# Kernel optimization log

Measured on AMD Instinct MI355X. Metric: run time of the kernel, lower is better.

Reference implementation:

```python
import jax, jax.numpy as jnp
import numpy as np

B, H, W, C = 32, 512, 512, 3


def dct2_matrix(N):
    # Orthonormal DCT-II basis: D[k, n] = s_k * sqrt(2/N) * cos(pi*(2n+1)*k/(2N))
    n = np.arange(N)
    k = n[:, None]
    D = np.cos(np.pi * (2 * n[None, :] + 1) * k / (2.0 * N)) * np.sqrt(2.0 / N)
    D[0, :] *= 1.0 / np.sqrt(2.0)  # ortho scaling of DC row
    return jnp.asarray(D, dtype=jnp.float32)


def setup_inputs() -> dict:
    key = jax.random.key(0)
    x = jax.random.normal(key, (B, H, W, C), dtype=jnp.float32)
    return {"x": x}


def reference(x) -> jnp.ndarray:
    # 2D DCT-II (ortho) along height and width, channels untouched.
    Dh = dct2_matrix(x.shape[1])  # [H, H]
    Dw = dct2_matrix(x.shape[2])  # [W, W]
    y = jnp.einsum('kh,bhwc->bkwc', Dh, x)   # DCT over height
    y = jnp.einsum('lw,bkwc->bklc', Dw, y)   # DCT over width
    return y
```

## Files before the change

### kernel.cpp

```cpp
#include <hip/hip_runtime.h>
#include <stdint.h>


typedef __bf16 bf16_t;
typedef bf16_t bf16x8 __attribute__((ext_vector_type(8)));
typedef float  f32x4  __attribute__((ext_vector_type(4)));

__device__ __forceinline__ uint32_t f2bf(float f) {
    union { float f; uint32_t u; } v; v.f = f;
    uint32_t r = v.u + 0x7fffu + ((v.u >> 16) & 1u);
    return r >> 16;
}

__device__ __forceinline__ f32x4 mfma16(bf16x8 a, bf16x8 b, f32x4 c) {
    return __builtin_amdgcn_mfma_f32_16x16x32_bf16(a, b, c, 0, 0, 0);
}

__device__ __forceinline__ void load_lds16(const void* g, void* l) {
    __builtin_amdgcn_global_load_lds(
        (const __attribute__((address_space(1))) uint32_t*)g,
        (__attribute__((address_space(3))) uint32_t*)l, 16, 0, 0);
}

__global__ __launch_bounds__(256) void gen_dct(uint16_t* __restrict__ Dbf) {
    int idx = blockIdx.x * 256 + threadIdx.x;
    int k = idx >> 9, h = idx & 511;
    int phase = ((2 * h + 1) * k) & 2047;
    float ang = (float)phase * 3.0679615757712823e-3f;
    float s = (k == 0) ? 0.04419417382415922f : 0.0625f;
    Dbf[idx] = (uint16_t)f2bf(__cosf(ang) * s);
}

__global__ __launch_bounds__(256, 3) void pass1(const float* __restrict__ x,
                                                const uint16_t* __restrict__ Dbf,
                                                uint16_t* __restrict__ Y) {
    __shared__ __align__(16) uint16_t Alds[128 * 32];
    __shared__ __align__(16) uint16_t Blds[96 * 32];
    const int t = threadIdx.x;
    const int lane = t & 63, wv = t >> 6;
    const int nt = blockIdx.x;
    const int mt = blockIdx.y;
    const int b  = blockIdx.z;
    const float* xb = x + (size_t)b * (512 * 1536);

    const int jl = t % 96;
    const int hh = t / 96;
    const int wl = jl / 3, cc = jl - 3 * wl;
    const int ncol = cc * 32 + ((wl >> 1) + ((wl & 1) << 4));
    const int xv = (ncol >> 1) & 3;
    const int jg = nt * 96 + jl;

    f32x4 acc[2][6] = {};

    for (int kt = 0; kt < 16; ++kt) {
        __syncthreads();
        {
            int q = t;
            load_lds16(Dbf + (size_t)(mt * 128 + (q >> 2)) * 512 + kt * 32 + (q & 3) * 8,
                       Alds + q * 8);
            int q2 = t + 256;
            load_lds16(Dbf + (size_t)(mt * 128 + (q2 >> 2)) * 512 + kt * 32 + (q2 & 3) * 8,
                       Alds + q2 * 8);
        }
        if (t < 192) {
            const float* src = xb + (size_t)(kt * 32 + hh * 16) * 1536 + jg;
            float v[16];
#pragma unroll
            for (int r = 0; r < 16; ++r) v[r] = src[(size_t)r * 1536];
            uint32_t p[8];
#pragma unroll
            for (int i = 0; i < 8; ++i)
                p[i] = f2bf(v[2 * i]) | (f2bf(v[2 * i + 1]) << 16);
            *(uint4*)&Blds[ncol * 32 + (((hh * 2 + 0) ^ xv) << 3)] =
                make_uint4(p[0], p[1], p[2], p[3]);
            *(uint4*)&Blds[ncol * 32 + (((hh * 2 + 1) ^ xv) << 3)] =
                make_uint4(p[4], p[5], p[6], p[7]);
        }
        __syncthreads();

        bf16x8 aq[2];
#pragma unroll
        for (int i = 0; i < 2; ++i)
            aq[i] = *(bf16x8*)&Alds[((wv * 2 + i) * 16 + (lane & 15)) * 32 + ((lane >> 4) << 3)];
#pragma unroll
        for (int tt = 0; tt < 6; ++tt) {
            int col = tt * 16 + (lane & 15);
            bf16x8 bq = *(bf16x8*)&Blds[col * 32 + (((lane >> 4) ^ ((col >> 1) & 3)) << 3)];
            acc[0][tt] = mfma16(aq[0], bq, acc[0][tt]);
            acc[1][tt] = mfma16(aq[1], bq, acc[1][tt]);
        }
    }

    const int wg = nt * 32 + 2 * (lane & 15);
#pragma unroll
    for (int i = 0; i < 2; ++i) {
        int kg = mt * 128 + (wv * 2 + i) * 16 + ((lane >> 4) << 2);
#pragma unroll
        for (int c = 0; c < 3; ++c)
#pragma unroll
            for (int r = 0; r < 4; ++r) {
                uint32_t pk = f2bf(acc[i][2 * c][r]) | (f2bf(acc[i][2 * c + 1][r]) << 16);
                *(uint32_t*)&Y[(size_t)b * 786432 + (size_t)(kg + r) * 1536 + c * 512 + wg] = pk;
            }
    }
}

__global__ __launch_bounds__(256, 3) void pass2(const uint16_t* __restrict__ Y,
                                                const uint16_t* __restrict__ Dbf,
                                                float* __restrict__ out) {
    __shared__ __align__(16) char smem[96 * 130 * 4];
    uint16_t* Alds = (uint16_t*)smem;
    uint16_t* Blds = (uint16_t*)(smem + 6144);
    float*    Elds = (float*)smem;
    const int t = threadIdx.x;
    const int lane = t & 63, wv = t >> 6;
    const int lt = blockIdx.x;
    const int mt = blockIdx.y;
    const int b  = blockIdx.z;
    const size_t yb = (size_t)b * 786432;

    f32x4 acc[6][2] = {};

    for (int kt = 0; kt < 16; ++kt) {
        __syncthreads();
        {
            int q = t;
            load_lds16(Y + yb + (size_t)(mt * 96 + (q >> 2)) * 512 + kt * 32 + (q & 3) * 8,
                       Alds + q * 8);
            if (t < 128) {
                int q2 = 256 + t;
                load_lds16(Y + yb + (size_t)(mt * 96 + (q2 >> 2)) * 512 + kt * 32 + (q2 & 3) * 8,
                           Alds + q2 * 8);
            }
            int q3 = t;
            load_lds16(Dbf + (size_t)(lt * 128 + (q3 >> 2)) * 512 + kt * 32 + (q3 & 3) * 8,
                       Blds + q3 * 8);
            int q4 = t + 256;
            load_lds16(Dbf + (size_t)(lt * 128 + (q4 >> 2)) * 512 + kt * 32 + (q4 & 3) * 8,
                       Blds + q4 * 8);
        }
        __syncthreads();

        bf16x8 bq[2];
#pragma unroll
        for (int p = 0; p < 2; ++p)
            bq[p] = *(bf16x8*)&Blds[((wv * 2 + p) * 16 + (lane & 15)) * 32 + ((lane >> 4) << 3)];
#pragma unroll
        for (int tt = 0; tt < 6; ++tt) {
            bf16x8 aq = *(bf16x8*)&Alds[(tt * 16 + (lane & 15)) * 32 + ((lane >> 4) << 3)];
            acc[tt][0] = mfma16(aq, bq[0], acc[tt][0]);
            acc[tt][1] = mfma16(aq, bq[1], acc[tt][1]);
        }
    }

    __syncthreads();
#pragma unroll
    for (int tt = 0; tt < 6; ++tt)
#pragma unroll
        for (int p = 0; p < 2; ++p) {
            int m = tt * 16 + ((lane >> 4) << 2);
            int ll = (wv * 2 + p) * 16 + (lane & 15);
#pragma unroll
            for (int r = 0; r < 4; ++r)
                Elds[(m + r) * 130 + ll] = acc[tt][p][r];
        }
    __syncthreads();

    const int kloc = t >> 3, sub = t & 7;
    size_t ob = (size_t)b * 786432 + (size_t)(mt * 32 + kloc) * 1536 + lt * 384 + sub * 48;
#pragma unroll
    for (int q = 0; q < 12; ++q) {
        int o0 = sub * 48 + q * 4;
        float4 v;
        v.x = Elds[(kloc * 3 + ((o0 + 0) % 3)) * 130 + (o0 + 0) / 3];
        v.y = Elds[(kloc * 3 + ((o0 + 1) % 3)) * 130 + (o0 + 1) / 3];
        v.z = Elds[(kloc * 3 + ((o0 + 2) % 3)) * 130 + (o0 + 2) / 3];
        v.w = Elds[(kloc * 3 + ((o0 + 3) % 3)) * 130 + (o0 + 3) / 3];
        *(float4*)&out[ob + q * 4] = v;
    }
}

extern "C" void kernel_launch(void* const* d_in, const int* in_sizes, int n_in,
                              void* d_out, int out_size, void* d_ws, size_t ws_size,
                              hipStream_t stream) {
    (void)in_sizes; (void)n_in; (void)out_size; (void)ws_size;
    const float* x = (const float*)d_in[0];
    float* out = (float*)d_out;
    uint16_t* Dbf = (uint16_t*)d_ws;
    uint16_t* Y   = (uint16_t*)d_ws + 512 * 512;

    gen_dct<<<1024, 256, 0, stream>>>(Dbf);
    dim3 g1(16, 4, 32);
    pass1<<<g1, 256, 0, stream>>>(x, Dbf, Y);
    dim3 g2(4, 16, 32);
    pass2<<<g2, 256, 0, stream>>>(Y, Dbf, out);
}
```

Baseline: 292.4 us.

## Double-buffer LDS tiles in both DCT GEMM passes with swizzled A loads

Both GEMM passes now keep two LDS buffers and prefetch the next K-tile while MFMAs run on the current one, so only one barrier per iteration remains. The global-to-LDS copies for the DCT matrix and Y tiles use an XOR swizzle to cut LDS bank conflicts on fragment reads. Pass2's epilogue is split into two halves so its staging area fits the smaller shared buffer, which allows occupancy to rise from 3 to 4 blocks. In exchange there is more register pressure from holding prefetched x values across the MFMA loop, and the epilogue needs extra barriers.

```diff
diff --git a/kernel.cpp b/kernel.cpp
--- a/kernel.cpp
+++ b/kernel.cpp
@@ -31,11 +31,11 @@
     Dbf[idx] = (uint16_t)f2bf(__cosf(ang) * s);
 }
 
-__global__ __launch_bounds__(256, 3) void pass1(const float* __restrict__ x,
+__global__ __launch_bounds__(256, 4) void pass1(const float* __restrict__ x,
                                                 const uint16_t* __restrict__ Dbf,
                                                 uint16_t* __restrict__ Y) {
-    __shared__ __align__(16) uint16_t Alds[128 * 32];
-    __shared__ __align__(16) uint16_t Blds[96 * 32];
+    __shared__ __align__(16) uint16_t Alds[2][128 * 32];
+    __shared__ __align__(16) uint16_t Blds[2][96 * 32];
     const int t = threadIdx.x;
     const int lane = t & 63, wv = t >> 6;
     const int nt = blockIdx.x;
@@ -43,52 +43,79 @@
     const int b  = blockIdx.z;
     const float* xb = x + (size_t)b * (512 * 1536);
 
+    const int q0 = t, q1 = t + 256;
+    const int m0 = q0 >> 2, i0 = (q0 & 3) ^ ((m0 >> 1) & 3);
+    const int m1 = q1 >> 2, i1 = (q1 & 3) ^ ((m1 >> 1) & 3);
+    const uint16_t* Asrc0 = Dbf + (size_t)(mt * 128 + m0) * 512 + i0 * 8;
+    const uint16_t* Asrc1 = Dbf + (size_t)(mt * 128 + m1) * 512 + i1 * 8;
+
     const int jl = t % 96;
     const int hh = t / 96;
     const int wl = jl / 3, cc = jl - 3 * wl;
     const int ncol = cc * 32 + ((wl >> 1) + ((wl & 1) << 4));
     const int xv = (ncol >> 1) & 3;
     const int jg = nt * 96 + jl;
+    const float* xsrc = xb + (size_t)(hh * 16) * 1536 + jg;
 
     f32x4 acc[2][6] = {};
+    float v[16];
+
+    load_lds16(Asrc0, &Alds[0][q0 * 8]);
+    load_lds16(Asrc1, &Alds[0][q1 * 8]);
+    if (t < 192) {
+#pragma unroll
+        for (int r = 0; r < 16; ++r) v[r] = xsrc[(size_t)r * 1536];
+        uint32_t p[8];
+#pragma unroll
+        for (int i = 0; i < 8; ++i)
+            p[i] = f2bf(v[2 * i]) | (f2bf(v[2 * i + 1]) << 16);
+        *(uint4*)&Blds[0][ncol * 32 + (((hh * 2 + 0) ^ xv) << 3)] =
+            make_uint4(p[0], p[1], p[2], p[3]);
+        *(uint4*)&Blds[0][ncol * 32 + (((hh * 2 + 1) ^ xv) << 3)] =
+            make_uint4(p[4], p[5], p[6], p[7]);
+    }
+    __syncthreads();
 
     for (int kt = 0; kt < 16; ++kt) {
-        __syncthreads();
-        {
-            int q = t;
-            load_lds16(Dbf + (size_t)(mt * 128 + (q >> 2)) * 512 + kt * 32 + (q & 3) * 8,
-                       Alds + q * 8);
-            int q2 = t + 256;
-            load_lds16(Dbf + (size_t)(mt * 128 + (q2 >> 2)) * 512 + kt * 32 + (q2 & 3) * 8,
-                       Alds + q2 * 8);
-        }
-        if (t < 192) {
-            const float* src = xb + (size_t)(kt * 32 + hh * 16) * 1536 + jg;
-            float v[16];
-#pragma unroll
-            for (int r = 0; r < 16; ++r) v[r] = src[(size_t)r * 1536];
+        const int cur = kt & 1, nxt = cur ^ 1;
+
+        if (kt < 15) {
+            load_lds16(Asrc0 + (kt + 1) * 32, &Alds[nxt][q0 * 8]);
+            load_lds16(Asrc1 + (kt + 1) * 32, &Alds[nxt][q1 * 8]);
+            if (t < 192) {
+                const float* s = xsrc + (size_t)(kt + 1) * 32 * 1536;
+#pragma unroll
+                for (int r = 0; r < 16; ++r) v[r] = s[(size_t)r * 1536];
+            }
+        }
+
+        bf16x8 aq[2];
+#pragma unroll
+        for (int i = 0; i < 2; ++i) {
+            int row = (wv * 2 + i) * 16 + (lane & 15);
+            aq[i] = *(bf16x8*)&Alds[cur][row * 32 +
+                        (((lane >> 4) ^ ((row >> 1) & 3)) << 3)];
+        }
+#pragma unroll
+        for (int tt = 0; tt < 6; ++tt) {
+            int col = tt * 16 + (lane & 15);
+            bf16x8 bq = *(bf16x8*)&Blds[cur][col * 32 +
+                        (((lane >> 4) ^ ((col >> 1) & 3)) << 3)];
+            acc[0][tt] = mfma16(aq[0], bq, acc[0][tt]);
+            acc[1][tt] = mfma16(aq[1], bq, acc[1][tt]);
+        }
+
+        if (kt < 15 && t < 192) {
             uint32_t p[8];
 #pragma unroll
             for (int i = 0; i < 8; ++i)
                 p[i] = f2bf(v[2 * i]) | (f2bf(v[2 * i + 1]) << 16);
-            *(uint4*)&Blds[ncol * 32 + (((hh * 2 + 0) ^ xv) << 3)] =
+            *(uint4*)&Blds[nxt][ncol * 32 + (((hh * 2 + 0) ^ xv) << 3)] =
                 make_uint4(p[0], p[1], p[2], p[3]);
-            *(uint4*)&Blds[ncol * 32 + (((hh * 2 + 1) ^ xv) << 3)] =
+            *(uint4*)&Blds[nxt][ncol * 32 + (((hh * 2 + 1) ^ xv) << 3)] =
                 make_uint4(p[4], p[5], p[6], p[7]);
         }
         __syncthreads();
-
-        bf16x8 aq[2];
-#pragma unroll
-        for (int i = 0; i < 2; ++i)
-            aq[i] = *(bf16x8*)&Alds[((wv * 2 + i) * 16 + (lane & 15)) * 32 + ((lane >> 4) << 3)];
-#pragma unroll
-        for (int tt = 0; tt < 6; ++tt) {
-            int col = tt * 16 + (lane & 15);
-            bf16x8 bq = *(bf16x8*)&Blds[col * 32 + (((lane >> 4) ^ ((col >> 1) & 3)) << 3)];
-            acc[0][tt] = mfma16(aq[0], bq, acc[0][tt]);
-            acc[1][tt] = mfma16(aq[1], bq, acc[1][tt]);
-        }
     }
 
     const int wg = nt * 32 + 2 * (lane & 15);
@@ -105,13 +132,10 @@
     }
 }
 
-__global__ __launch_bounds__(256, 3) void pass2(const uint16_t* __restrict__ Y,
+__global__ __launch_bounds__(256, 4) void pass2(const uint16_t* __restrict__ Y,
                                                 const uint16_t* __restrict__ Dbf,
                                                 float* __restrict__ out) {
-    __shared__ __align__(16) char smem[96 * 130 * 4];
-    uint16_t* Alds = (uint16_t*)smem;
-    uint16_t* Blds = (uint16_t*)(smem + 6144);
-    float*    Elds = (float*)smem;
+    __shared__ __align__(16) char smem[28672];
     const int t = threadIdx.x;
     const int lane = t & 63, wv = t >> 6;
     const int lt = blockIdx.x;
@@ -119,64 +143,87 @@
     const int b  = blockIdx.z;
     const size_t yb = (size_t)b * 786432;
 
+    const int qa0 = t;
+    const int ma0 = qa0 >> 2, ia0 = (qa0 & 3) ^ ((ma0 >> 1) & 3);
+    const int qa1 = t + 256;
+    const int ma1 = qa1 >> 2, ia1 = (qa1 & 3) ^ ((ma1 >> 1) & 3);
+    const int mb0 = ma0, ib0 = ia0;
+    const int mb1 = ma1, ib1 = ia1;
+
+    const uint16_t* As0 = Y + yb + (size_t)(mt * 96 + ma0) * 512 + ia0 * 8;
+    const uint16_t* As1 = Y + yb + (size_t)(mt * 96 + ma1) * 512 + ia1 * 8;
+    const uint16_t* Bs0 = Dbf + (size_t)(lt * 128 + mb0) * 512 + ib0 * 8;
+    const uint16_t* Bs1 = Dbf + (size_t)(lt * 128 + mb1) * 512 + ib1 * 8;
+
     f32x4 acc[6][2] = {};
 
+    auto stage = [&](int kt, int buf) {
+        uint16_t* Al = (uint16_t*)(smem + buf * 14336);
+        uint16_t* Bl = (uint16_t*)(smem + buf * 14336 + 6144);
+        load_lds16(As0 + kt * 32, Al + qa0 * 8);
+        if (t < 128) load_lds16(As1 + kt * 32, Al + qa1 * 8);
+        load_lds16(Bs0 + kt * 32, Bl + qa0 * 8);
+        load_lds16(Bs1 + kt * 32, Bl + qa1 * 8);
+    };
+
+    stage(0, 0);
+    __syncthreads();
+
     for (int kt = 0; kt < 16; ++kt) {
-        __syncthreads();
-        {
-            int q = t;
-            load_lds16(Y + yb + (size_t)(mt * 96 + (q >> 2)) * 512 + kt * 32 + (q & 3) * 8,
-                       Alds + q * 8);
-            if (t < 128) {
-                int q2 = 256 + t;
-                load_lds16(Y + yb + (size_t)(mt * 96 + (q2 >> 2)) * 512 + kt * 32 + (q2 & 3) * 8,
-                           Alds + q2 * 8);
-            }
-            int q3 = t;
-            load_lds16(Dbf + (size_t)(lt * 128 + (q3 >> 2)) * 512 + kt * 32 + (q3 & 3) * 8,
-                       Blds + q3 * 8);
-            int q4 = t + 256;
-            load_lds16(Dbf + (size_t)(lt * 128 + (q4 >> 2)) * 512 + kt * 32 + (q4 & 3) * 8,
-                       Blds + q4 * 8);
-        }
-        __syncthreads();
+        const int cur = kt & 1;
+        if (kt < 15) stage(kt + 1, cur ^ 1);
+
+        const uint16_t* Al = (const uint16_t*)(smem + cur * 14336);
+        const uint16_t* Bl = (const uint16_t*)(smem + cur * 14336 + 6144);
 
         bf16x8 bq[2];
 #pragma unroll
-        for (int p = 0; p < 2; ++p)
-            bq[p] = *(bf16x8*)&Blds[((wv * 2 + p) * 16 + (lane & 15)) * 32 + ((lane >> 4) << 3)];
+        for (int p = 0; p < 2; ++p) {
+            int row = (wv * 2 + p) * 16 + (lane & 15);
+            bq[p] = *(bf16x8*)&Bl[row * 32 +
+                        (((lane >> 4) ^ ((row >> 1) & 3)) << 3)];
+        }
 #pragma unroll
         for (int tt = 0; tt < 6; ++tt) {
-            bf16x8 aq = *(bf16x8*)&Alds[(tt * 16 + (lane & 15)) * 32 + ((lane >> 4) << 3)];
+            int row = tt * 16 + (lane & 15);
+            bf16x8 aq = *(bf16x8*)&Al[row * 32 +
+                        (((lane >> 4) ^ ((row >> 1) & 3)) << 3)];
             acc[tt][0] = mfma16(aq, bq[0], acc[tt][0]);
             acc[tt][1] = mfma16(aq, bq[1], acc[tt][1]);
         }
-    }
-
-    __syncthreads();
-#pragma unroll
-    for (int tt = 0; tt < 6; ++tt)
-#pragma unroll
-        for (int p = 0; p < 2; ++p) {
-            int m = tt * 16 + ((lane >> 4) << 2);
-            int ll = (wv * 2 + p) * 16 + (lane & 15);
-#pragma unroll
-            for (int r = 0; r < 4; ++r)
-                Elds[(m + r) * 130 + ll] = acc[tt][p][r];
-        }
-    __syncthreads();
-
+        __syncthreads();
+    }
+
+    float* El = (float*)smem;
     const int kloc = t >> 3, sub = t & 7;
-    size_t ob = (size_t)b * 786432 + (size_t)(mt * 32 + kloc) * 1536 + lt * 384 + sub * 48;
-#pragma unroll
-    for (int q = 0; q < 12; ++q) {
-        int o0 = sub * 48 + q * 4;
-        float4 v;
-        v.x = Elds[(kloc * 3 + ((o0 + 0) % 3)) * 130 + (o0 + 0) / 3];
-        v.y = Elds[(kloc * 3 + ((o0 + 1) % 3)) * 130 + (o0 + 1) / 3];
-        v.z = Elds[(kloc * 3 + ((o0 + 2) % 3)) * 130 + (o0 + 2) / 3];
-        v.w = Elds[(kloc * 3 + ((o0 + 3) % 3)) * 130 + (o0 + 3) / 3];
-        *(float4*)&out[ob + q * 4] = v;
+#pragma unroll
+    for (int hf = 0; hf < 2; ++hf) {
+        __syncthreads();
+        if ((wv >> 1) == hf) {
+#pragma unroll
+            for (int tt = 0; tt < 6; ++tt)
+#pragma unroll
+                for (int p = 0; p < 2; ++p) {
+                    int m = tt * 16 + ((lane >> 4) << 2);
+                    int lc = ((wv & 1) * 2 + p) * 16 + (lane & 15);
+#pragma unroll
+                    for (int r = 0; r < 4; ++r)
+                        El[(m + r) * 65 + lc] = acc[tt][p][r];
+                }
+        }
+        __syncthreads();
+        size_t ob = (size_t)b * 786432 + (size_t)(mt * 32 + kloc) * 1536 +
+                    lt * 384 + hf * 192 + sub * 24;
+#pragma unroll
+        for (int q = 0; q < 6; ++q) {
+            int o0 = hf * 192 + sub * 24 + q * 4;
+            float4 v;
+            v.x = El[(kloc * 3 + ((o0 + 0) % 3)) * 65 + ((o0 + 0) / 3 - hf * 64)];
+            v.y = El[(kloc * 3 + ((o0 + 1) % 3)) * 65 + ((o0 + 1) / 3 - hf * 64)];
+            v.z = El[(kloc * 3 + ((o0 + 2) % 3)) * 65 + ((o0 + 2) / 3 - hf * 64)];
+            v.w = El[(kloc * 3 + ((o0 + 3) % 3)) * 65 + ((o0 + 3) / 3 - hf * 64)];
+            *(float4*)&out[ob + q * 4] = v;
+        }
     }
 }
 
```

Result: faster. 277.6 us (-5.1%).

## Double output tile per block in both DCT passes and swizzle LDS operands

Applied to the files above, without the earlier changes.

Each block of pass1 and pass2 now computes two 128-row tiles of the DCT basis output instead of one, so every loaded tile of x (pass1) or Y (pass2) is reused across twice as many MFMAs. The grid shrinks by half in the tiled dimension. XOR swizzles are added to the A/B LDS layouts to cut bank conflicts, and load addresses are hoisted out of the k loop. Pass2's epilogue is split into four smaller LDS staging rounds to fit the smaller shared buffer. The cost is doubled accumulator registers, which may lower occupancy, and fewer blocks in flight.

```diff
diff --git a/kernel.cpp b/kernel.cpp
--- a/kernel.cpp
+++ b/kernel.cpp
@@ -34,36 +34,43 @@
 __global__ __launch_bounds__(256, 3) void pass1(const float* __restrict__ x,
                                                 const uint16_t* __restrict__ Dbf,
                                                 uint16_t* __restrict__ Y) {
-    __shared__ __align__(16) uint16_t Alds[128 * 32];
+    __shared__ __align__(16) uint16_t Alds[256 * 32];
     __shared__ __align__(16) uint16_t Blds[96 * 32];
     const int t = threadIdx.x;
     const int lane = t & 63, wv = t >> 6;
     const int nt = blockIdx.x;
-    const int mt = blockIdx.y;
+    const int mp = blockIdx.y;
     const int b  = blockIdx.z;
     const float* xb = x + (size_t)b * (512 * 1536);
+
+    const int q0 = t, q1 = t + 256, q2 = t + 512, q3 = t + 768;
+    const int m0 = q0 >> 2, i0 = (q0 & 3) ^ ((m0 >> 1) & 3);
+    const int m1 = q1 >> 2, i1 = (q1 & 3) ^ ((m1 >> 1) & 3);
+    const int m2 = q2 >> 2, i2 = (q2 & 3) ^ ((m2 >> 1) & 3);
+    const int m3 = q3 >> 2, i3 = (q3 & 3) ^ ((m3 >> 1) & 3);
+    const uint16_t* As0 = Dbf + (size_t)(mp * 256 + m0) * 512 + i0 * 8;
+    const uint16_t* As1 = Dbf + (size_t)(mp * 256 + m1) * 512 + i1 * 8;
+    const uint16_t* As2 = Dbf + (size_t)(mp * 256 + m2) * 512 + i2 * 8;
+    const uint16_t* As3 = Dbf + (size_t)(mp * 256 + m3) * 512 + i3 * 8;
 
     const int jl = t % 96;
     const int hh = t / 96;
     const int wl = jl / 3, cc = jl - 3 * wl;
     const int ncol = cc * 32 + ((wl >> 1) + ((wl & 1) << 4));
-    const int xv = (ncol >> 1) & 3;
+    const int xv = ((ncol >> 1) ^ (ncol >> 3) ^ (ncol >> 5)) & 3;
     const int jg = nt * 96 + jl;
-
-    f32x4 acc[2][6] = {};
+    const float* xsrc = xb + (size_t)(hh * 16) * 1536 + jg;
+
+    f32x4 acc[2][2][6] = {};
 
     for (int kt = 0; kt < 16; ++kt) {
         __syncthreads();
-        {
-            int q = t;
-            load_lds16(Dbf + (size_t)(mt * 128 + (q >> 2)) * 512 + kt * 32 + (q & 3) * 8,
-                       Alds + q * 8);
-            int q2 = t + 256;
-            load_lds16(Dbf + (size_t)(mt * 128 + (q2 >> 2)) * 512 + kt * 32 + (q2 & 3) * 8,
-                       Alds + q2 * 8);
-        }
+        load_lds16(As0 + kt * 32, Alds + q0 * 8);
+        load_lds16(As1 + kt * 32, Alds + q1 * 8);
+        load_lds16(As2 + kt * 32, Alds + q2 * 8);
+        load_lds16(As3 + kt * 32, Alds + q3 * 8);
         if (t < 192) {
-            const float* src = xb + (size_t)(kt * 32 + hh * 16) * 1536 + jg;
+            const float* src = xsrc + (size_t)kt * 32 * 1536;
             float v[16];
 #pragma unroll
             for (int r = 0; r < 16; ++r) v[r] = src[(size_t)r * 1536];
@@ -78,105 +85,140 @@
         }
         __syncthreads();
 
-        bf16x8 aq[2];
-#pragma unroll
-        for (int i = 0; i < 2; ++i)
-            aq[i] = *(bf16x8*)&Alds[((wv * 2 + i) * 16 + (lane & 15)) * 32 + ((lane >> 4) << 3)];
+        bf16x8 aq[2][2];
+#pragma unroll
+        for (int mtk = 0; mtk < 2; ++mtk)
+#pragma unroll
+            for (int i = 0; i < 2; ++i) {
+                int row = mtk * 128 + (wv * 2 + i) * 16 + (lane & 15);
+                aq[mtk][i] = *(const bf16x8*)&Alds[row * 32 +
+                                (((lane >> 4) ^ ((row >> 1) & 3)) << 3)];
+            }
 #pragma unroll
         for (int tt = 0; tt < 6; ++tt) {
             int col = tt * 16 + (lane & 15);
-            bf16x8 bq = *(bf16x8*)&Blds[col * 32 + (((lane >> 4) ^ ((col >> 1) & 3)) << 3)];
-            acc[0][tt] = mfma16(aq[0], bq, acc[0][tt]);
-            acc[1][tt] = mfma16(aq[1], bq, acc[1][tt]);
+            int xr = ((col >> 1) ^ (col >> 3) ^ (col >> 5)) & 3;
+            bf16x8 bq = *(const bf16x8*)&Blds[col * 32 + (((lane >> 4) ^ xr) << 3)];
+#pragma unroll
+            for (int mtk = 0; mtk < 2; ++mtk) {
+                acc[mtk][0][tt] = mfma16(aq[mtk][0], bq, acc[mtk][0][tt]);
+                acc[mtk][1][tt] = mfma16(aq[mtk][1], bq, acc[mtk][1][tt]);
+            }
         }
     }
 
     const int wg = nt * 32 + 2 * (lane & 15);
 #pragma unroll
-    for (int i = 0; i < 2; ++i) {
-        int kg = mt * 128 + (wv * 2 + i) * 16 + ((lane >> 4) << 2);
-#pragma unroll
-        for (int c = 0; c < 3; ++c)
-#pragma unroll
-            for (int r = 0; r < 4; ++r) {
-                uint32_t pk = f2bf(acc[i][2 * c][r]) | (f2bf(acc[i][2 * c + 1][r]) << 16);
-                *(uint32_t*)&Y[(size_t)b * 786432 + (size_t)(kg + r) * 1536 + c * 512 + wg] = pk;
-            }
-    }
+    for (int mtk = 0; mtk < 2; ++mtk)
+#pragma unroll
+        for (int i = 0; i < 2; ++i) {
+            int kg = mp * 256 + mtk * 128 + (wv * 2 + i) * 16 + ((lane >> 4) << 2);
+#pragma unroll
+            for (int c = 0; c < 3; ++c)
+#pragma unroll
+                for (int r = 0; r < 4; ++r) {
+                    uint32_t pk = f2bf(acc[mtk][i][2 * c][r]) |
+                                  (f2bf(acc[mtk][i][2 * c + 1][r]) << 16);
+                    *(uint32_t*)&Y[(size_t)b * 786432 + (size_t)(kg + r) * 1536 +
+                                   c * 512 + wg] = pk;
+                }
+        }
 }
 
 __global__ __launch_bounds__(256, 3) void pass2(const uint16_t* __restrict__ Y,
                                                 const uint16_t* __restrict__ Dbf,
                                                 float* __restrict__ out) {
-    __shared__ __align__(16) char smem[96 * 130 * 4];
+    __shared__ __align__(16) char smem[24960];
     uint16_t* Alds = (uint16_t*)smem;
     uint16_t* Blds = (uint16_t*)(smem + 6144);
-    float*    Elds = (float*)smem;
+    float*    El   = (float*)smem;
     const int t = threadIdx.x;
     const int lane = t & 63, wv = t >> 6;
-    const int lt = blockIdx.x;
+    const int lp = blockIdx.x;
     const int mt = blockIdx.y;
     const int b  = blockIdx.z;
     const size_t yb = (size_t)b * 786432;
 
-    f32x4 acc[6][2] = {};
+    const int q0 = t, q1 = t + 256, q2 = t + 512, q3 = t + 768;
+    const int m0 = q0 >> 2, i0 = (q0 & 3) ^ ((m0 >> 1) & 3);
+    const int m1 = q1 >> 2, i1 = (q1 & 3) ^ ((m1 >> 1) & 3);
+    const int m2 = q2 >> 2, i2 = (q2 & 3) ^ ((m2 >> 1) & 3);
+    const int m3 = q3 >> 2, i3 = (q3 & 3) ^ ((m3 >> 1) & 3);
+
+    const uint16_t* Ys0 = Y + yb + (size_t)(mt * 96 + m0) * 512 + i0 * 8;
+    const uint16_t* Ys1 = Y + yb + (size_t)(mt * 96 + m1) * 512 + i1 * 8;
+    const uint16_t* Ds0 = Dbf + (size_t)(lp * 256 + m0) * 512 + i0 * 8;
+    const uint16_t* Ds1 = Dbf + (size_t)(lp * 256 + m1) * 512 + i1 * 8;
+    const uint16_t* Ds2 = Dbf + (size_t)(lp * 256 + m2) * 512 + i2 * 8;
+    const uint16_t* Ds3 = Dbf + (size_t)(lp * 256 + m3) * 512 + i3 * 8;
+
+    f32x4 acc[6][2][2] = {};
 
     for (int kt = 0; kt < 16; ++kt) {
         __syncthreads();
-        {
-            int q = t;
-            load_lds16(Y + yb + (size_t)(mt * 96 + (q >> 2)) * 512 + kt * 32 + (q & 3) * 8,
-                       Alds + q * 8);
-            if (t < 128) {
-                int q2 = 256 + t;
-                load_lds16(Y + yb + (size_t)(mt * 96 + (q2 >> 2)) * 512 + kt * 32 + (q2 & 3) * 8,
-                           Alds + q2 * 8);
-            }
-            int q3 = t;
-            load_lds16(Dbf + (size_t)(lt * 128 + (q3 >> 2)) * 512 + kt * 32 + (q3 & 3) * 8,
-                       Blds + q3 * 8);
-            int q4 = t + 256;
-            load_lds16(Dbf + (size_t)(lt * 128 + (q4 >> 2)) * 512 + kt * 32 + (q4 & 3) * 8,
-                       Blds + q4 * 8);
-        }
-        __syncthreads();
-
-        bf16x8 bq[2];
-#pragma unroll
-        for (int p = 0; p < 2; ++p)
-            bq[p] = *(bf16x8*)&Blds[((wv * 2 + p) * 16 + (lane & 15)) * 32 + ((lane >> 4) << 3)];
+        load_lds16(Ys0 + kt * 32, Alds + q0 * 8);
+        if (t < 128) load_lds16(Ys1 + kt * 32, Alds + q1 * 8);
+        load_lds16(Ds0 + kt * 32, Blds + q0 * 8);
+        load_lds16(Ds1 + kt * 32, Blds + q1 * 8);
+        load_lds16(Ds2 + kt * 32, Blds + q2 * 8);
+        load_lds16(Ds3 + kt * 32, Blds + q3 * 8);
+        __syncthreads();
+
+        bf16x8 bq[2][2];
+#pragma unroll
+        for (int lt2 = 0; lt2 < 2; ++lt2)
+#pragma unroll
+            for (int p = 0; p < 2; ++p) {
+                int row = lt2 * 128 + (wv * 2 + p) * 16 + (lane & 15);
+                bq[lt2][p] = *(const bf16x8*)&Blds[row * 32 +
+                                (((lane >> 4) ^ ((row >> 1) & 3)) << 3)];
+            }
 #pragma unroll
         for (int tt = 0; tt < 6; ++tt) {
-            bf16x8 aq = *(bf16x8*)&Alds[(tt * 16 + (lane & 15)) * 32 + ((lane >> 4) << 3)];
-            acc[tt][0] = mfma16(aq, bq[0], acc[tt][0]);
-            acc[tt][1] = mfma16(aq, bq[1], acc[tt][1]);
+            int row = tt * 16 + (lane & 15);
+            bf16x8 aq = *(const bf16x8*)&Alds[row * 32 +
+                            (((lane >> 4) ^ ((row >> 1) & 3)) << 3)];
+#pragma unroll
+            for (int lt2 = 0; lt2 < 2; ++lt2) {
+                acc[tt][0][lt2] = mfma16(aq, bq[lt2][0], acc[tt][0][lt2]);
+                acc[tt][1][lt2] = mfma16(aq, bq[lt2][1], acc[tt][1][lt2]);
+            }
         }
     }
 
-    __syncthreads();
-#pragma unroll
-    for (int tt = 0; tt < 6; ++tt)
-#pragma unroll
-        for (int p = 0; p < 2; ++p) {
-            int m = tt * 16 + ((lane >> 4) << 2);
-            int ll = (wv * 2 + p) * 16 + (lane & 15);
-#pragma unroll
-            for (int r = 0; r < 4; ++r)
-                Elds[(m + r) * 130 + ll] = acc[tt][p][r];
-        }
-    __syncthreads();
-
     const int kloc = t >> 3, sub = t & 7;
-    size_t ob = (size_t)b * 786432 + (size_t)(mt * 32 + kloc) * 1536 + lt * 384 + sub * 48;
-#pragma unroll
-    for (int q = 0; q < 12; ++q) {
-        int o0 = sub * 48 + q * 4;
-        float4 v;
-        v.x = Elds[(kloc * 3 + ((o0 + 0) % 3)) * 130 + (o0 + 0) / 3];
-        v.y = Elds[(kloc * 3 + ((o0 + 1) % 3)) * 130 + (o0 + 1) / 3];
-        v.z = Elds[(kloc * 3 + ((o0 + 2) % 3)) * 130 + (o0 + 2) / 3];
-        v.w = Elds[(kloc * 3 + ((o0 + 3) % 3)) * 130 + (o0 + 3) / 3];
-        *(float4*)&out[ob + q * 4] = v;
+#pragma unroll
+    for (int lt2 = 0; lt2 < 2; ++lt2) {
+        const int lte = lp * 2 + lt2;
+#pragma unroll
+        for (int hf = 0; hf < 2; ++hf) {
+            __syncthreads();
+            if ((wv >> 1) == hf) {
+#pragma unroll
+                for (int tt = 0; tt < 6; ++tt)
+#pragma unroll
+                    for (int p = 0; p < 2; ++p) {
+                        int m = tt * 16 + ((lane >> 4) << 2);
+                        int lc = ((wv & 1) * 2 + p) * 16 + (lane & 15);
+#pragma unroll
+                        for (int r = 0; r < 4; ++r)
+                            El[(m + r) * 65 + lc] = acc[tt][p][lt2][r];
+                    }
+            }
+            __syncthreads();
+            size_t ob = (size_t)b * 786432 + (size_t)(mt * 32 + kloc) * 1536 +
+                        lte * 384 + hf * 192 + sub * 24;
+#pragma unroll
+            for (int q = 0; q < 6; ++q) {
+                int o0 = hf * 192 + sub * 24 + q * 4;
+                float4 v;
+                v.x = El[(kloc * 3 + ((o0 + 0) % 3)) * 65 + ((o0 + 0) / 3 - hf * 64)];
+                v.y = El[(kloc * 3 + ((o0 + 1) % 3)) * 65 + ((o0 + 1) / 3 - hf * 64)];
+                v.z = El[(kloc * 3 + ((o0 + 2) % 3)) * 65 + ((o0 + 2) / 3 - hf * 64)];
+                v.w = El[(kloc * 3 + ((o0 + 3) % 3)) * 65 + ((o0 + 3) / 3 - hf * 64)];
+                *(float4*)&out[ob + q * 4] = v;
+            }
+        }
     }
 }
 
@@ -190,8 +232,8 @@
     uint16_t* Y   = (uint16_t*)d_ws + 512 * 512;
 
     gen_dct<<<1024, 256, 0, stream>>>(Dbf);
-    dim3 g1(16, 4, 32);
+    dim3 g1(16, 2, 32);
     pass1<<<g1, 256, 0, stream>>>(x, Dbf, Y);
-    dim3 g2(4, 16, 32);
+    dim3 g2(2, 16, 32);
     pass2<<<g2, 256, 0, stream>>>(Y, Dbf, out);
 }
```

New measurement: 292.5 us. About the same (+0.0%).

## Split fp32-to-bf16 transpose out of GEMM1 and enlarge MFMA tiles to 512 threads

Applied to the files above, without the earlier changes.

Adds a separate transpose kernel that converts x to bf16 and lays it out with height contiguous, so the first GEMM can stream both operands with direct global-to-LDS loads. Both GEMMs move to 512-thread blocks with larger tiles (128x256 and 96x256), a K-step of 64 and XOR-swizzled LDS. The output epilogue is staged in two rounds through LDS. The extra transpose kernel adds a full read and write of the input plus another launch, and Xt falls back to aliasing the output buffer when the workspace is too small.

```diff
diff --git a/kernel.cpp b/kernel.cpp
--- a/kernel.cpp
+++ b/kernel.cpp
@@ -31,167 +31,220 @@
     Dbf[idx] = (uint16_t)f2bf(__cosf(ang) * s);
 }
 
-__global__ __launch_bounds__(256, 3) void pass1(const float* __restrict__ x,
+__global__ __launch_bounds__(256) void xpose(const float* __restrict__ x,
+                                             uint16_t* __restrict__ Xt) {
+    const int jt = blockIdx.x, hb = blockIdx.y, b = blockIdx.z;
+    const int t = threadIdx.x;
+    const int jl = t & 127, hh = t >> 7;
+    const int jg = jt * 128 + jl;
+    const int w = jg / 3, c = jg - 3 * w;
+    const int wr = ((w >> 8) << 8) + ((w & 255) >> 1) + ((w & 1) << 7);
+    const int jr = c * 512 + wr;
+    const float* src = x + (size_t)b * 786432 +
+                       (size_t)(hb * 32 + hh * 16) * 1536 + jg;
+    float v[16];
+#pragma unroll
+    for (int r = 0; r < 16; ++r) v[r] = src[(size_t)r * 1536];
+    uint32_t p[8];
+#pragma unroll
+    for (int i = 0; i < 8; ++i)
+        p[i] = f2bf(v[2 * i]) | (f2bf(v[2 * i + 1]) << 16);
+    size_t dst = ((size_t)b * 1536 + jr) * 512 + hb * 32 + hh * 16;
+    *(uint4*)&Xt[dst]     = make_uint4(p[0], p[1], p[2], p[3]);
+    *(uint4*)&Xt[dst + 8] = make_uint4(p[4], p[5], p[6], p[7]);
+}
+
+__global__ __launch_bounds__(512, 2) void gemm1(const uint16_t* __restrict__ Xt,
                                                 const uint16_t* __restrict__ Dbf,
                                                 uint16_t* __restrict__ Y) {
-    __shared__ __align__(16) uint16_t Alds[128 * 32];
-    __shared__ __align__(16) uint16_t Blds[96 * 32];
+    __shared__ __align__(16) uint16_t Al[128 * 64];
+    __shared__ __align__(16) uint16_t Bl[256 * 64];
     const int t = threadIdx.x;
     const int lane = t & 63, wv = t >> 6;
+    const int wm = wv >> 2, wn = wv & 3;
     const int nt = blockIdx.x;
     const int mt = blockIdx.y;
     const int b  = blockIdx.z;
-    const float* xb = x + (size_t)b * (512 * 1536);
-
-    const int jl = t % 96;
-    const int hh = t / 96;
-    const int wl = jl / 3, cc = jl - 3 * wl;
-    const int ncol = cc * 32 + ((wl >> 1) + ((wl & 1) << 4));
-    const int xv = (ncol >> 1) & 3;
-    const int jg = nt * 96 + jl;
-
-    f32x4 acc[2][6] = {};
-
-    for (int kt = 0; kt < 16; ++kt) {
-        __syncthreads();
-        {
-            int q = t;
-            load_lds16(Dbf + (size_t)(mt * 128 + (q >> 2)) * 512 + kt * 32 + (q & 3) * 8,
-                       Alds + q * 8);
-            int q2 = t + 256;
-            load_lds16(Dbf + (size_t)(mt * 128 + (q2 >> 2)) * 512 + kt * 32 + (q2 & 3) * 8,
-                       Alds + q2 * 8);
-        }
-        if (t < 192) {
-            const float* src = xb + (size_t)(kt * 32 + hh * 16) * 1536 + jg;
-            float v[16];
-#pragma unroll
-            for (int r = 0; r < 16; ++r) v[r] = src[(size_t)r * 1536];
-            uint32_t p[8];
-#pragma unroll
-            for (int i = 0; i < 8; ++i)
-                p[i] = f2bf(v[2 * i]) | (f2bf(v[2 * i + 1]) << 16);
-            *(uint4*)&Blds[ncol * 32 + (((hh * 2 + 0) ^ xv) << 3)] =
-                make_uint4(p[0], p[1], p[2], p[3]);
-            *(uint4*)&Blds[ncol * 32 + (((hh * 2 + 1) ^ xv) << 3)] =
-                make_uint4(p[4], p[5], p[6], p[7]);
-        }
-        __syncthreads();
-
-        bf16x8 aq[2];
-#pragma unroll
-        for (int i = 0; i < 2; ++i)
-            aq[i] = *(bf16x8*)&Alds[((wv * 2 + i) * 16 + (lane & 15)) * 32 + ((lane >> 4) << 3)];
-#pragma unroll
-        for (int tt = 0; tt < 6; ++tt) {
-            int col = tt * 16 + (lane & 15);
-            bf16x8 bq = *(bf16x8*)&Blds[col * 32 + (((lane >> 4) ^ ((col >> 1) & 3)) << 3)];
-            acc[0][tt] = mfma16(aq[0], bq, acc[0][tt]);
-            acc[1][tt] = mfma16(aq[1], bq, acc[1][tt]);
-        }
-    }
-
-    const int wg = nt * 32 + 2 * (lane & 15);
-#pragma unroll
-    for (int i = 0; i < 2; ++i) {
-        int kg = mt * 128 + (wv * 2 + i) * 16 + ((lane >> 4) << 2);
-#pragma unroll
-        for (int c = 0; c < 3; ++c)
+
+    const int qa0 = t, qa1 = t + 512;
+    const int ma0 = qa0 >> 3, ga0 = (qa0 & 7) ^ (ma0 & 7);
+    const int ma1 = qa1 >> 3, ga1 = (qa1 & 7) ^ (ma1 & 7);
+    const uint16_t* As0 = Dbf + (size_t)(mt * 128 + ma0) * 512 + ga0 * 8;
+    const uint16_t* As1 = Dbf + (size_t)(mt * 128 + ma1) * 512 + ga1 * 8;
+    const uint16_t* Bs[4];
+    int qb[4];
+#pragma unroll
+    for (int i = 0; i < 4; ++i) {
+        qb[i] = t + 512 * i;
+        int mb = qb[i] >> 3, gb = (qb[i] & 7) ^ (mb & 7);
+        Bs[i] = Xt + ((size_t)b * 1536 + nt * 256 + mb) * 512 + gb * 8;
+    }
+
+    f32x4 acc[4][4] = {};
+
+    for (int kt = 0; kt < 8; ++kt) {
+        __syncthreads();
+        load_lds16(As0 + kt * 64, Al + qa0 * 8);
+        load_lds16(As1 + kt * 64, Al + qa1 * 8);
+#pragma unroll
+        for (int i = 0; i < 4; ++i)
+            load_lds16(Bs[i] + kt * 64, Bl + qb[i] * 8);
+        __syncthreads();
+
+#pragma unroll
+        for (int ks = 0; ks < 2; ++ks) {
+            bf16x8 aq[4], bq[4];
+#pragma unroll
+            for (int mf = 0; mf < 4; ++mf) {
+                int row = wm * 64 + mf * 16 + (lane & 15);
+                int sl = (ks * 4 + (lane >> 4)) ^ (row & 7);
+                aq[mf] = *(const bf16x8*)&Al[row * 64 + sl * 8];
+            }
+#pragma unroll
+            for (int f = 0; f < 4; ++f) {
+                int col = (wn + 4 * f) * 16 + (lane & 15);
+                int sl = (ks * 4 + (lane >> 4)) ^ (col & 7);
+                bq[f] = *(const bf16x8*)&Bl[col * 64 + sl * 8];
+            }
+#pragma unroll
+            for (int mf = 0; mf < 4; ++mf)
+#pragma unroll
+                for (int f = 0; f < 4; ++f)
+                    acc[mf][f] = mfma16(aq[mf], bq[f], acc[mf][f]);
+        }
+    }
+
+    const int cch = nt >> 1, whalf = nt & 1;
+#pragma unroll
+    for (int mf = 0; mf < 4; ++mf)
+#pragma unroll
+        for (int fp = 0; fp < 2; ++fp) {
+            int kbase = mt * 128 + wm * 64 + mf * 16 + ((lane >> 4) << 2);
+            int u = wn + 4 * fp;
+            int w = whalf * 256 + 2 * (u * 16 + (lane & 15));
 #pragma unroll
             for (int r = 0; r < 4; ++r) {
-                uint32_t pk = f2bf(acc[i][2 * c][r]) | (f2bf(acc[i][2 * c + 1][r]) << 16);
-                *(uint32_t*)&Y[(size_t)b * 786432 + (size_t)(kg + r) * 1536 + c * 512 + wg] = pk;
-            }
-    }
-}
-
-__global__ __launch_bounds__(256, 3) void pass2(const uint16_t* __restrict__ Y,
+                uint32_t pk = f2bf(acc[mf][fp][r]) |
+                              (f2bf(acc[mf][fp + 2][r]) << 16);
+                *(uint32_t*)&Y[(size_t)b * 786432 + (size_t)(kbase + r) * 1536 +
+                               cch * 512 + w] = pk;
+            }
+        }
+}
+
+__global__ __launch_bounds__(512, 4) void gemm2(const uint16_t* __restrict__ Y,
                                                 const uint16_t* __restrict__ Dbf,
                                                 float* __restrict__ out) {
-    __shared__ __align__(16) char smem[96 * 130 * 4];
-    uint16_t* Alds = (uint16_t*)smem;
-    uint16_t* Blds = (uint16_t*)(smem + 6144);
-    float*    Elds = (float*)smem;
+    __shared__ __align__(16) char smem[49408];
+    uint16_t* Al = (uint16_t*)smem;
+    uint16_t* Bl = (uint16_t*)(smem + 12288);
+    float*    El = (float*)smem;
     const int t = threadIdx.x;
     const int lane = t & 63, wv = t >> 6;
-    const int lt = blockIdx.x;
-    const int mt = blockIdx.y;
+    const int wm = wv >> 2, wn = wv & 3;
+    const int mt = blockIdx.x;
+    const int lt = blockIdx.y;
     const int b  = blockIdx.z;
     const size_t yb = (size_t)b * 786432;
 
-    f32x4 acc[6][2] = {};
-
-    for (int kt = 0; kt < 16; ++kt) {
-        __syncthreads();
-        {
-            int q = t;
-            load_lds16(Y + yb + (size_t)(mt * 96 + (q >> 2)) * 512 + kt * 32 + (q & 3) * 8,
-                       Alds + q * 8);
-            if (t < 128) {
-                int q2 = 256 + t;
-                load_lds16(Y + yb + (size_t)(mt * 96 + (q2 >> 2)) * 512 + kt * 32 + (q2 & 3) * 8,
-                           Alds + q2 * 8);
-            }
-            int q3 = t;
-            load_lds16(Dbf + (size_t)(lt * 128 + (q3 >> 2)) * 512 + kt * 32 + (q3 & 3) * 8,
-                       Blds + q3 * 8);
-            int q4 = t + 256;
-            load_lds16(Dbf + (size_t)(lt * 128 + (q4 >> 2)) * 512 + kt * 32 + (q4 & 3) * 8,
-                       Blds + q4 * 8);
-        }
-        __syncthreads();
-
-        bf16x8 bq[2];
-#pragma unroll
-        for (int p = 0; p < 2; ++p)
-            bq[p] = *(bf16x8*)&Blds[((wv * 2 + p) * 16 + (lane & 15)) * 32 + ((lane >> 4) << 3)];
-#pragma unroll
-        for (int tt = 0; tt < 6; ++tt) {
-            bf16x8 aq = *(bf16x8*)&Alds[(tt * 16 + (lane & 15)) * 32 + ((lane >> 4) << 3)];
-            acc[tt][0] = mfma16(aq, bq[0], acc[tt][0]);
-            acc[tt][1] = mfma16(aq, bq[1], acc[tt][1]);
-        }
-    }
-
-    __syncthreads();
-#pragma unroll
-    for (int tt = 0; tt < 6; ++tt)
-#pragma unroll
-        for (int p = 0; p < 2; ++p) {
-            int m = tt * 16 + ((lane >> 4) << 2);
-            int ll = (wv * 2 + p) * 16 + (lane & 15);
-#pragma unroll
-            for (int r = 0; r < 4; ++r)
-                Elds[(m + r) * 130 + ll] = acc[tt][p][r];
-        }
-    __syncthreads();
-
-    const int kloc = t >> 3, sub = t & 7;
-    size_t ob = (size_t)b * 786432 + (size_t)(mt * 32 + kloc) * 1536 + lt * 384 + sub * 48;
-#pragma unroll
-    for (int q = 0; q < 12; ++q) {
-        int o0 = sub * 48 + q * 4;
-        float4 v;
-        v.x = Elds[(kloc * 3 + ((o0 + 0) % 3)) * 130 + (o0 + 0) / 3];
-        v.y = Elds[(kloc * 3 + ((o0 + 1) % 3)) * 130 + (o0 + 1) / 3];
-        v.z = Elds[(kloc * 3 + ((o0 + 2) % 3)) * 130 + (o0 + 2) / 3];
-        v.w = Elds[(kloc * 3 + ((o0 + 3) % 3)) * 130 + (o0 + 3) / 3];
-        *(float4*)&out[ob + q * 4] = v;
+    const int qa0 = t, qa1 = t + 512;
+    const int ma0 = qa0 >> 3, ga0 = (qa0 & 7) ^ (ma0 & 7);
+    const int ma1 = qa1 >> 3, ga1 = (qa1 & 7) ^ (ma1 & 7);
+    const uint16_t* As0 = Y + yb + (size_t)(mt * 96 + ma0) * 512 + ga0 * 8;
+    const uint16_t* As1 = Y + yb + (size_t)(mt * 96 + ma1) * 512 + ga1 * 8;
+    const uint16_t* Bs[4];
+    int qb[4];
+#pragma unroll
+    for (int i = 0; i < 4; ++i) {
+        qb[i] = t + 512 * i;
+        int mb = qb[i] >> 3, gb = (qb[i] & 7) ^ (mb & 7);
+        Bs[i] = Dbf + (size_t)(lt * 256 + mb) * 512 + gb * 8;
+    }
+
+    f32x4 acc[3][4] = {};
+
+    for (int kt = 0; kt < 8; ++kt) {
+        __syncthreads();
+        load_lds16(As0 + kt * 64, Al + qa0 * 8);
+        if (t < 256) load_lds16(As1 + kt * 64, Al + qa1 * 8);
+#pragma unroll
+        for (int i = 0; i < 4; ++i)
+            load_lds16(Bs[i] + kt * 64, Bl + qb[i] * 8);
+        __syncthreads();
+
+#pragma unroll
+        for (int ks = 0; ks < 2; ++ks) {
+            bf16x8 aq[3], bq[4];
+#pragma unroll
+            for (int mf = 0; mf < 3; ++mf) {
+                int row = wm * 48 + mf * 16 + (lane & 15);
+                int sl = (ks * 4 + (lane >> 4)) ^ (row & 7);
+                aq[mf] = *(const bf16x8*)&Al[row * 64 + sl * 8];
+            }
+#pragma unroll
+            for (int f = 0; f < 4; ++f) {
+                int col = wn * 64 + f * 16 + (lane & 15);
+                int sl = (ks * 4 + (lane >> 4)) ^ (col & 7);
+                bq[f] = *(const bf16x8*)&Bl[col * 64 + sl * 8];
+            }
+#pragma unroll
+            for (int mf = 0; mf < 3; ++mf)
+#pragma unroll
+                for (int f = 0; f < 4; ++f)
+                    acc[mf][f] = mfma16(aq[mf], bq[f], acc[mf][f]);
+        }
+    }
+
+    const int kloc = t >> 5, zrow = t & 31;
+#pragma unroll
+    for (int rnd = 0; rnd < 2; ++rnd) {
+        __syncthreads();
+        if (wm == rnd) {
+#pragma unroll
+            for (int mf = 0; mf < 3; ++mf)
+#pragma unroll
+                for (int f = 0; f < 4; ++f) {
+                    int row = mf * 16 + ((lane >> 4) << 2);
+                    int col = wn * 64 + f * 16 + (lane & 15);
+#pragma unroll
+                    for (int r = 0; r < 4; ++r)
+                        El[(row + r) * 257 + col] = acc[mf][f][r];
+                }
+        }
+        __syncthreads();
+        int kbase = mt * 32 + rnd * 16;
+        size_t ob = (size_t)b * 786432 + (size_t)(kbase + kloc) * 1536 + lt * 768;
+#pragma unroll
+        for (int q4 = 0; q4 < 6; ++q4) {
+            int z0 = zrow * 24 + q4 * 4;
+            float4 v;
+            v.x = El[(kloc * 3 + ((z0 + 0) % 3)) * 257 + (z0 + 0) / 3];
+            v.y = El[(kloc * 3 + ((z0 + 1) % 3)) * 257 + (z0 + 1) / 3];
+            v.z = El[(kloc * 3 + ((z0 + 2) % 3)) * 257 + (z0 + 2) / 3];
+            v.w = El[(kloc * 3 + ((z0 + 3) % 3)) * 257 + (z0 + 3) / 3];
+            *(float4*)&out[ob + z0] = v;
+        }
     }
 }
 
 extern "C" void kernel_launch(void* const* d_in, const int* in_sizes, int n_in,
                               void* d_out, int out_size, void* d_ws, size_t ws_size,
                               hipStream_t stream) {
-    (void)in_sizes; (void)n_in; (void)out_size; (void)ws_size;
+    (void)in_sizes; (void)n_in; (void)out_size;
     const float* x = (const float*)d_in[0];
     float* out = (float*)d_out;
     uint16_t* Dbf = (uint16_t*)d_ws;
-    uint16_t* Y   = (uint16_t*)d_ws + 512 * 512;
+    uint16_t* Yw  = (uint16_t*)d_ws + 512 * 512;
+    size_t need = (size_t)512 * 512 * 2 + (size_t)2 * 32 * 1536 * 512 * 2;
+    uint16_t* Xt = (ws_size >= need)
+                     ? (uint16_t*)d_ws + 512 * 512 + (size_t)32 * 1536 * 512
+                     : (uint16_t*)d_out;
 
     gen_dct<<<1024, 256, 0, stream>>>(Dbf);
-    dim3 g1(16, 4, 32);
-    pass1<<<g1, 256, 0, stream>>>(x, Dbf, Y);
-    dim3 g2(4, 16, 32);
-    pass2<<<g2, 256, 0, stream>>>(Y, Dbf, out);
-}
+    dim3 gt(12, 16, 32);
+    xpose<<<gt, 256, 0, stream>>>(x, Xt);
+    dim3 g1(6, 4, 32);
+    gemm1<<<g1, 512, 0, stream>>>(Xt, Dbf, Yw);
+    dim3 g2(16, 2, 32);
+    gemm2<<<g2, 512, 0, stream>>>(Yw, Dbf, out);
+}
```

After: 278.6 us. 1.05x faster.
